# Performance work log

Measured on AMD Instinct MI355X. Metric: run time of the kernel, lower is better.

The kernel has to match this reference:

```python
import jax, jax.numpy as jnp
import numpy as np

D = 128        # node_state_dim
F = 10         # len(CHOSEN_CONNECTION_FEATURES)
N_IP = 20000
N_CONN = 100000
E = 200000
T = 3


def _seg_mean(vals, ids, n):
    s = jax.ops.segment_sum(vals, ids, num_segments=n)
    c = jax.ops.segment_sum(jnp.ones((vals.shape[0], 1), vals.dtype), ids, num_segments=n)
    return s / jnp.maximum(c, 1.0)


def _gru(x, h, kernel, rec_kernel, bias):
    # keras GRUCell, reset_after=True, gate order [z, r, hh]
    xm = x @ kernel + bias[0]
    hm = h @ rec_kernel + bias[1]
    xz, xr, xh = jnp.split(xm, 3, axis=-1)
    hz, hr, hh = jnp.split(hm, 3, axis=-1)
    z = jax.nn.sigmoid(xz + hz)
    r = jax.nn.sigmoid(xr + hr)
    hcand = jnp.tanh(xh + r * hh)
    return z * h + (1.0 - z) * hcand


def setup_inputs() -> dict:
    key = jax.random.key(0)
    ks = jax.random.split(key, 24)
    s = 0.02
    inp = {
        "feature_connection": jax.random.normal(ks[0], (N_CONN, F), jnp.float32),
        "src_ip_to_connection": jax.random.randint(ks[1], (E,), 0, N_IP, jnp.int32),
        "dst_ip_to_connection": jax.random.randint(ks[2], (E,), 0, N_CONN, jnp.int32),
        "src_connection_to_ip": jax.random.randint(ks[3], (E,), 0, N_CONN, jnp.int32),
        "dst_connection_to_ip": jax.random.randint(ks[4], (E,), 0, N_IP, jnp.int32),
        # message MLPs
        "W_m1": jax.random.normal(ks[5], (2 * D, D), jnp.float32) * s,
        "b_m1": jnp.zeros((D,), jnp.float32),
        "W_m2": jax.random.normal(ks[6], (2 * D, D), jnp.float32) * s,
        "b_m2": jnp.zeros((D,), jnp.float32),
        # GRU cells
        "gru_ip_k": jax.random.normal(ks[7], (D, 3 * D), jnp.float32) * s,
        "gru_ip_r": jax.random.normal(ks[8], (D, 3 * D), jnp.float32) * s,
        "gru_ip_b": jnp.zeros((2, 3 * D), jnp.float32),
        "gru_c_k": jax.random.normal(ks[9], (D, 3 * D), jnp.float32) * s,
        "gru_c_r": jax.random.normal(ks[10], (D, 3 * D), jnp.float32) * s,
        "gru_c_b": jnp.zeros((2, 3 * D), jnp.float32),
        # readout MLP
        "W_r1": jax.random.normal(ks[11], (D, 128), jnp.float32) * s,
        "b_r1": jnp.zeros((128,), jnp.float32),
        "W_r2": jax.random.normal(ks[12], (128, 64), jnp.float32) * s,
        "b_r2": jnp.zeros((64,), jnp.float32),
        "W_r3": jax.random.normal(ks[13], (64, 15), jnp.float32) * s,
        "b_r3": jnp.zeros((15,), jnp.float32),
    }
    return inp


def reference(feature_connection, src_ip_to_connection, dst_ip_to_connection,
              src_connection_to_ip, dst_connection_to_ip,
              W_m1, b_m1, W_m2, b_m2,
              gru_ip_k, gru_ip_r, gru_ip_b,
              gru_c_k, gru_c_r, gru_c_b,
              W_r1, b_r1, W_r2, b_r2, W_r3, b_r3):
    ip_state = jnp.ones((N_IP, D), jnp.float32)
    connection_state = jnp.concatenate(
        [feature_connection, jnp.zeros((N_CONN, D - F), jnp.float32)], axis=1)

    for _ in range(T):
        # ip -> connection messages
        nn_in = jnp.concatenate([ip_state[src_ip_to_connection],
                                 connection_state[dst_ip_to_connection]], axis=1)
        ip_message = jax.nn.relu(nn_in @ W_m1 + b_m1)            # [E, D]
        ip_mean = _seg_mean(ip_message, dst_ip_to_connection, N_CONN)
        # connection -> ip messages
        nn_in2 = jnp.concatenate([connection_state[src_connection_to_ip],
                                  ip_state[dst_connection_to_ip]], axis=1)
        conn_message = jax.nn.relu(nn_in2 @ W_m2 + b_m2)         # [E, D]
        conn_mean = _seg_mean(conn_message, dst_connection_to_ip, N_IP)
        # GRU updates
        ip_state = _gru(conn_mean, ip_state, gru_ip_k, gru_ip_r, gru_ip_b)
        connection_state = _gru(ip_mean, connection_state, gru_c_k, gru_c_r, gru_c_b)

    h = jax.nn.relu(connection_state @ W_r1 + b_r1)
    h = jax.nn.relu(h @ W_r2 + b_r2)
    return jax.nn.softmax(h @ W_r3 + b_r3, axis=-1)              # [N_CONN, 15]
```

## Files before the change

kernel.cpp:

```cpp
#include <hip/hip_runtime.h>
#include <math.h>

#define D 128
#define NF 10
#define N_IP 20000
#define N_CONN 100000
#define NE 200000
#define T_ROUNDS 3

typedef unsigned short u16;
using bf16x8 = __attribute__((ext_vector_type(8))) short;
using floatx4 = __attribute__((ext_vector_type(4))) float;

__device__ inline u16 f2bf(float f) {
  union { float f; unsigned u; } v; v.f = f;
  unsigned u = v.u;
  return (u16)((u + 0x7fffu + ((u >> 16) & 1u)) >> 16);
}
__device__ inline float bf2f(u16 h) {
  union { unsigned u; float f; } v; v.u = ((unsigned)h) << 16; return v.f;
}
__device__ __forceinline__ unsigned cvtpk(float lo, float hi) {
  unsigned r;
  asm("v_cvt_pk_bf16_f32 %0, %1, %2" : "=v"(r) : "v"(lo), "v"(hi));
  return r;
}

__device__ inline float fsigmoid(float s) { return 1.f / (1.f + __expf(-s)); }
__device__ inline float ftanh(float a) {
  a = fminf(fmaxf(a, -15.f), 15.f);
  float e = __expf(2.f * a);
  return (e - 1.f) / (e + 1.f);
}

__device__ __forceinline__ void gld16(const u16* g, u16* l) {
  __builtin_amdgcn_global_load_lds(
      (const __attribute__((address_space(1))) unsigned int*)g,
      (__attribute__((address_space(3))) unsigned int*)l, 16, 0, 0);
}

__global__ void k_setup(u16* __restrict__ ip_state, u16* __restrict__ conn_state,
                        const float* __restrict__ feat, int* __restrict__ cnt,
                        const float* __restrict__ gik, const float* __restrict__ gir,
                        const float* __restrict__ gck, const float* __restrict__ gcr,
                        const float* __restrict__ Wm1, const float* __restrict__ Wm2,
                        const float* __restrict__ Wr1, const float* __restrict__ Wr2,
                        u16* __restrict__ gikb, u16* __restrict__ girb,
                        u16* __restrict__ gckb, u16* __restrict__ gcrb,
                        u16* __restrict__ wm1b, u16* __restrict__ wm2b,
                        u16* __restrict__ wm1t, u16* __restrict__ wm2t,
                        u16* __restrict__ wr1b, u16* __restrict__ wr2b,
                        float* __restrict__ csum) {
  int i = blockIdx.x * blockDim.x + threadIdx.x;
  const int nip = N_IP * D;
  const int nstate = (N_IP + N_CONN) * D;
  if (i < nip) {
    ip_state[i] = 0x3F80;
  } else if (i < nstate) {
    int j = i - nip;
    int r = j >> 7, c = j & 127;
    conn_state[j] = (c < NF) ? f2bf(feat[r * NF + c]) : (u16)0;
  }
  if (i < N_CONN + N_IP) cnt[i] = 0;
  if (i < 196608) {
    int m = i / 49152, r = i % 49152;
    const float* W = (m == 0) ? gik : (m == 1) ? gir : (m == 2) ? gck : gcr;
    u16* Wb = (m == 0) ? gikb : (m == 1) ? girb : (m == 2) ? gckb : gcrb;
    int col = r >> 7, k = r & 127;
    Wb[r] = f2bf(W[k * 384 + col]);
  } else if (i < 278528) {
    int j = i - 196608;
    int m = j / 16384, r = j % 16384;
    const float* W; u16* Wb; int k0;
    if (m == 0) { W = Wm1; Wb = wm1b; k0 = 128; }
    else if (m == 1) { W = Wm2; Wb = wm2b; k0 = 128; }
    else if (m == 2) { W = Wm1; Wb = wm1t; k0 = 0; }
    else if (m == 3) { W = Wm2; Wb = wm2t; k0 = 0; }
    else { W = Wr1; Wb = wr1b; k0 = 0; }
    int col = r >> 7, k = r & 127;
    Wb[r] = f2bf(W[(k0 + k) * 128 + col]);
  } else if (i < 286720) {
    int r = i - 278528;
    int col = r >> 7, k = r & 127;
    wr2b[r] = f2bf(Wr2[k * 64 + col]);
  } else if (i < 286848) {
    int c = i - 286720;
    float s = 0.f;
    for (int k = 0; k < 128; k++) s += Wm1[k * 128 + c];
    csum[c] = s;
  }
}

__global__ void k_initP_count(const float* __restrict__ csum, const float* __restrict__ feat,
                              const float* __restrict__ Wm2,
                              u16* __restrict__ P1, u16* __restrict__ P2,
                              const int* __restrict__ d1, const int* __restrict__ d2,
                              int* __restrict__ c1, int* __restrict__ c2) {
  int i = blockIdx.x * blockDim.x + threadIdx.x;
  if (i < NE) {
    atomicAdd(&c1[d1[i]], 1);
    atomicAdd(&c2[d2[i]], 1);
  }
  const int n1 = N_IP * 16;
  const int n2 = N_CONN * 16;
  if (i < n1) {
    int r = i >> 4, g = i & 15;
    u16 v[8];
#pragma unroll
    for (int k = 0; k < 8; k++) v[k] = f2bf(csum[g * 8 + k]);
    *(uint4*)(P1 + (size_t)r * 128 + g * 8) = *(const uint4*)v;
  } else if (i < n1 + n2) {
    int j = i - n1;
    int r = j >> 4, g = j & 15;
    float acc[8] = {0.f, 0.f, 0.f, 0.f, 0.f, 0.f, 0.f, 0.f};
#pragma unroll
    for (int k = 0; k < NF; k++) {
      float f = feat[(size_t)r * NF + k];
      const float* wrow = Wm2 + (size_t)k * 128 + g * 8;
#pragma unroll
      for (int c = 0; c < 8; c++) acc[c] += f * wrow[c];
    }
    u16 v[8];
#pragma unroll
    for (int c = 0; c < 8; c++) v[c] = f2bf(acc[c]);
    *(uint4*)(P2 + (size_t)r * 128 + g * 8) = *(const uint4*)v;
  }
}

__global__ void k_scan_part2(const int* __restrict__ cnt1, int* __restrict__ bsum1,
                             int n1, int nb1,
                             const int* __restrict__ cnt2, int* __restrict__ bsum2, int n2) {
  const int* cnt; int* bsum; int n, b;
  if ((int)blockIdx.x < nb1) { cnt = cnt1; bsum = bsum1; n = n1; b = blockIdx.x; }
  else { cnt = cnt2; bsum = bsum2; n = n2; b = blockIdx.x - nb1; }
  int t = threadIdx.x;
  int base = b * 1024 + t * 4;
  int s = 0;
#pragma unroll
  for (int i = 0; i < 4; i++) { int j = base + i; if (j < n) s += cnt[j]; }
  for (int d = 32; d > 0; d >>= 1) s += __shfl_xor(s, d, 64);
  __shared__ int wred[4];
  int lane = t & 63, wv = t >> 6;
  if (lane == 0) wred[wv] = s;
  __syncthreads();
  if (t == 0) bsum[b] = wred[0] + wred[1] + wred[2] + wred[3];
}

__device__ inline void scan_mid_body(int* bsum, int m, int t) {
  int v = (t < m) ? bsum[t] : 0;
  int lane = t & 63, wv = t >> 6;
  int x = v;
  for (int d = 1; d < 64; d <<= 1) { int y = __shfl_up(x, d, 64); if (lane >= d) x += y; }
  __shared__ int wsum[4];
  if (lane == 63) wsum[wv] = x;
  __syncthreads();
  int add = 0;
  for (int i = 0; i < wv; i++) add += wsum[i];
  int ex = add + x - v;
  if (t < m) bsum[t] = ex;
  __syncthreads();
}

__global__ void k_scan_mid2(int* __restrict__ bsum1, int m1, int* __restrict__ bsum2, int m2) {
  int t = threadIdx.x;
  scan_mid_body(bsum1, m1, t);
  scan_mid_body(bsum2, m2, t);
}

__global__ void k_scan_final2(const int* __restrict__ cnt1, const int* __restrict__ bsum1,
                              int* __restrict__ off1, int* __restrict__ cur1, int n1, int nb1,
                              const int* __restrict__ cnt2, const int* __restrict__ bsum2,
                              int* __restrict__ off2, int* __restrict__ cur2, int n2) {
  const int* cnt; const int* bsum; int* off; int* cur; int n, b;
  if ((int)blockIdx.x < nb1) {
    cnt = cnt1; bsum = bsum1; off = off1; cur = cur1; n = n1; b = blockIdx.x;
  } else {
    cnt = cnt2; bsum = bsum2; off = off2; cur = cur2; n = n2; b = blockIdx.x - nb1;
  }
  int t = threadIdx.x;
  int base = b * 1024 + t * 4;
  int vals[4]; int s = 0;
#pragma unroll
  for (int i = 0; i < 4; i++) {
    int j = base + i;
    vals[i] = (j < n) ? cnt[j] : 0;
    s += vals[i];
  }
  int lane = t & 63, wv = t >> 6;
  int x = s;
  for (int d = 1; d < 64; d <<= 1) { int y = __shfl_up(x, d, 64); if (lane >= d) x += y; }
  __shared__ int wsum[4];
  if (lane == 63) wsum[wv] = x;
  __syncthreads();
  int add = 0;
  for (int i = 0; i < wv; i++) add += wsum[i];
  int run = add + x - s + bsum[b];
#pragma unroll
  for (int i = 0; i < 4; i++) {
    int j = base + i;
    if (j < n) { off[j] = run; cur[j] = run; }
    run += vals[i];
  }
}

__global__ void k_scatter(const int* __restrict__ s1, const int* __restrict__ d1,
                          const int* __restrict__ s2, const int* __restrict__ d2,
                          int* __restrict__ cur1, int* __restrict__ cur2,
                          int* __restrict__ o1, int* __restrict__ o2) {
  int e = blockIdx.x * blockDim.x + threadIdx.x;
  if (e >= NE) return;
  int p1 = atomicAdd(&cur1[d1[e]], 1);
  o1[p1] = s1[e];
  int p2 = atomicAdd(&cur2[d2[e]], 1);
  o2[p2] = s2[e];
}

__global__ __launch_bounds__(512, 4) void k_msggru(
    u16* __restrict__ st1, const u16* __restrict__ wq1, const float* __restrict__ qb1,
    const u16* __restrict__ P1g, const int* __restrict__ srcs1g,
    const int* __restrict__ off1g, const int* __restrict__ cnt1g,
    const u16* __restrict__ wx1, const u16* __restrict__ wh1, const float* __restrict__ gb1,
    const u16* __restrict__ wp1, u16* __restrict__ Pn1, int r1, int tiles1,
    u16* __restrict__ st2, const u16* __restrict__ wq2, const float* __restrict__ qb2,
    const u16* __restrict__ P2g, const int* __restrict__ srcs2g,
    const int* __restrict__ off2g, const int* __restrict__ cnt2g,
    const u16* __restrict__ wx2, const u16* __restrict__ wh2, const float* __restrict__ gb2,
    const u16* __restrict__ wp2, u16* __restrict__ Pn2, int r2, int doP) {
  __shared__ __align__(16) char smem[65536];
  u16* Wls = (u16*)smem;
  u16* Qb = (u16*)smem;
  u16* bufA = (u16*)smem;
  u16* bufB = (u16*)(smem + 12288);
  u16* Hls = (u16*)(smem + 32768);
  u16* H; const u16* Wqb; const float* qbias; const u16* P;
  const int* srcs; const int* off; const int* cnt;
  const u16* Wxb; const u16* Whb; const float* gbias;
  const u16* Wpt; u16* Pn; int rows, bm;
  if ((int)blockIdx.x < tiles1) {
    H = st1; Wqb = wq1; qbias = qb1; P = P1g; srcs = srcs1g; off = off1g; cnt = cnt1g;
    Wxb = wx1; Whb = wh1; gbias = gb1; Wpt = wp1; Pn = Pn1; rows = r1; bm = blockIdx.x * 128;
  } else {
    H = st2; Wqb = wq2; qbias = qb2; P = P2g; srcs = srcs2g; off = off2g; cnt = cnt2g;
    Wxb = wx2; Whb = wh2; gbias = gb2; Wpt = wp2; Pn = Pn2; rows = r2;
    bm = (blockIdx.x - tiles1) * 128;
  }
  const int tid = threadIdx.x, wv = tid >> 6, lane = tid & 63;
  const int lrow = lane & 15, quad = lane >> 4;
#pragma unroll
  for (int j = 0; j < 4; j++) {
    int c = j * 512 + tid;
    int row = c >> 4, sl = c & 15;
    gld16(Wqb + (size_t)row * 128 + ((sl ^ (row & 15)) * 8), Wls + (size_t)c * 8);
  }
#pragma unroll
  for (int i = 0; i < 4; i++) {
    int c = i * 512 + tid;
    int row = c >> 4, sl = c & 15;
    gld16(H + (size_t)(bm + row) * 128 + ((sl ^ (row & 15)) * 8), Hls + (size_t)c * 8);
  }
  int oArr[4], nArr[4];
#pragma unroll
  for (int it = 0; it < 4; it++) {
    int nl = (it * 512 + tid) >> 4;
    int node = bm + nl;
    oArr[it] = (node < rows) ? off[node] : 0;
    nArr[it] = (node < rows) ? cnt[node] : 0;
  }
  __syncthreads();
  bf16x8 ah[4];
#pragma unroll
  for (int ks = 0; ks < 4; ks++)
    ah[ks] = *(const bf16x8*)(Hls + (size_t)(wv * 16 + lrow) * 128 + (((ks * 4 + quad) ^ lrow) * 8));
  floatx4 acc[8];
#pragma unroll
  for (int ct = 0; ct < 8; ct++) acc[ct] = {0.f, 0.f, 0.f, 0.f};
#pragma unroll
  for (int ks = 0; ks < 4; ks++) {
#pragma unroll
    for (int ct = 0; ct < 8; ct++) {
      bf16x8 b = *(const bf16x8*)(Wls + (size_t)(ct * 16 + lrow) * 128 + (((4 * ks + quad) ^ lrow) * 8));
      acc[ct] = __builtin_amdgcn_mfma_f32_16x16x32_bf16(ah[ks], b, acc[ct], 0, 0, 0);
    }
  }
  __syncthreads();
  {
    const int lr = wv * 16 + quad * 4;
#pragma unroll
    for (int ct = 0; ct < 8; ct++) {
      int col = ct * 16 + lrow;
      float bv = qbias[col];
      unsigned p01 = cvtpk(acc[ct][0] + bv, acc[ct][1] + bv);
      unsigned p23 = cvtpk(acc[ct][2] + bv, acc[ct][3] + bv);
      Qb[(size_t)(lr + 0) * 128 + col] = (u16)p01;
      Qb[(size_t)(lr + 1) * 128 + col] = (u16)(p01 >> 16);
      Qb[(size_t)(lr + 2) * 128 + col] = (u16)p23;
      Qb[(size_t)(lr + 3) * 128 + col] = (u16)(p23 >> 16);
    }
  }
  __syncthreads();
#pragma unroll
  for (int it = 0; it < 4; it++) {
    int task = it * 512 + tid;
    int nl = task >> 4, g = task & 15;
    int node = bm + nl;
    if (node >= rows) continue;
    int c8 = g << 3;
    float q[8];
    {
      uint4 qv = *(const uint4*)(Qb + (size_t)nl * 128 + c8);
      unsigned qq[4] = {qv.x, qv.y, qv.z, qv.w};
#pragma unroll
      for (int k = 0; k < 4; k++) {
        q[2 * k] = __uint_as_float(qq[k] << 16);
        q[2 * k + 1] = __uint_as_float(qq[k] & 0xffff0000u);
      }
    }
    float acg[8] = {0.f, 0.f, 0.f, 0.f, 0.f, 0.f, 0.f, 0.f};
    int o = oArr[it], n = nArr[it];
    for (int i = 0; i < n; i += 4) {
      int rem = n - i;
      int s0 = srcs[o + i];
      int s1 = srcs[o + i + (rem > 1 ? 1 : 0)];
      int s2 = srcs[o + i + (rem > 2 ? 2 : 0)];
      int s3 = srcs[o + i + (rem > 3 ? 3 : 0)];
      uint4 v0 = *(const uint4*)(P + (size_t)s0 * 128 + c8);
      uint4 v1 = *(const uint4*)(P + (size_t)s1 * 128 + c8);
      uint4 v2 = *(const uint4*)(P + (size_t)s2 * 128 + c8);
      uint4 v3 = *(const uint4*)(P + (size_t)s3 * 128 + c8);
      unsigned w[16] = {v0.x, v0.y, v0.z, v0.w, v1.x, v1.y, v1.z, v1.w,
                        v2.x, v2.y, v2.z, v2.w, v3.x, v3.y, v3.z, v3.w};
#pragma unroll
      for (int e = 0; e < 4; e++) {
        bool val = (e == 0) || (rem > e);
#pragma unroll
        for (int k = 0; k < 4; k++) {
          unsigned ww = w[e * 4 + k];
          float lo = __uint_as_float(ww << 16);
          float hi = __uint_as_float(ww & 0xffff0000u);
          float t0 = fmaxf(lo + q[2 * k], 0.f);
          float t1 = fmaxf(hi + q[2 * k + 1], 0.f);
          if (val) { acg[2 * k] += t0; acg[2 * k + 1] += t1; }
        }
      }
    }
    float inv = 1.f / fmaxf((float)n, 1.f);
    uint4 ov;
    ov.x = cvtpk(acg[0] * inv, acg[1] * inv);
    ov.y = cvtpk(acg[2] * inv, acg[3] * inv);
    ov.z = cvtpk(acg[4] * inv, acg[5] * inv);
    ov.w = cvtpk(acg[6] * inv, acg[7] * inv);
    *(uint4*)(Qb + (size_t)nl * 128 + ((g ^ (nl & 15)) * 8)) = ov;
  }
  __syncthreads();
  bf16x8 ax[4];
#pragma unroll
  for (int ks = 0; ks < 4; ks++)
    ax[ks] = *(const bf16x8*)(Qb + (size_t)(wv * 16 + lrow) * 128 + (((ks * 4 + quad) ^ lrow) * 8));
  const int lr0 = wv * 16 + quad * 4;
  __syncthreads();
#pragma unroll
  for (int j = 0; j < 2; j++) {
    int c = j * 512 + tid;
    if (c < 768) {
      int gate = c >> 8, colw = (c >> 4) & 15, sl = c & 15;
      gld16(Wxb + (size_t)(gate * 128 + 0 * 16 + colw) * 128 + ((sl ^ colw) * 8),
            bufA + (size_t)c * 8);
    }
  }
  for (int ch = 0; ch < 8; ch++) {
    __syncthreads();
#pragma unroll
    for (int j = 0; j < 2; j++) {
      int c = j * 512 + tid;
      if (c < 768) {
        int gate = c >> 8, colw = (c >> 4) & 15, sl = c & 15;
        gld16(Whb + (size_t)(gate * 128 + ch * 16 + colw) * 128 + ((sl ^ colw) * 8),
              bufB + (size_t)c * 8);
      }
    }
    floatx4 gacc[3][2];
#pragma unroll
    for (int g = 0; g < 3; g++) {
      gacc[g][0] = {0.f, 0.f, 0.f, 0.f};
      gacc[g][1] = {0.f, 0.f, 0.f, 0.f};
    }
#pragma unroll
    for (int ks = 0; ks < 4; ks++) {
      int posu = ((4 * ks + quad) ^ lrow) * 8;
#pragma unroll
      for (int g = 0; g < 3; g++) {
        bf16x8 bx = *(const bf16x8*)(bufA + (size_t)(g * 16 + lrow) * 128 + posu);
        gacc[g][0] = __builtin_amdgcn_mfma_f32_16x16x32_bf16(ax[ks], bx, gacc[g][0], 0, 0, 0);
      }
    }
    __syncthreads();
    if (ch < 7) {
#pragma unroll
      for (int j = 0; j < 2; j++) {
        int c = j * 512 + tid;
        if (c < 768) {
          int gate = c >> 8, colw = (c >> 4) & 15, sl = c & 15;
          gld16(Wxb + (size_t)(gate * 128 + (ch + 1) * 16 + colw) * 128 + ((sl ^ colw) * 8),
                bufA + (size_t)c * 8);
        }
      }
    }
#pragma unroll
    for (int ks = 0; ks < 4; ks++) {
      int posu = ((4 * ks + quad) ^ lrow) * 8;
#pragma unroll
      for (int g = 0; g < 3; g++) {
        bf16x8 bh = *(const bf16x8*)(bufB + (size_t)(g * 16 + lrow) * 128 + posu);
        gacc[g][1] = __builtin_amdgcn_mfma_f32_16x16x32_bf16(ah[ks], bh, gacc[g][1], 0, 0, 0);
      }
    }
    int hcol = ch * 16 + lrow;
    float bxz = gbias[hcol];
    float bxr = gbias[128 + hcol];
    float bxh = gbias[256 + hcol];
    float bhz = gbias[384 + hcol];
    float bhr = gbias[384 + 128 + hcol];
    float bhh = gbias[384 + 256 + hcol];
    int ggr = 2 * ch + (lrow >> 3);
    int gel = lrow & 7;
    float hn[4];
#pragma unroll
    for (int reg = 0; reg < 4; reg++) {
      int lr = lr0 + reg;
      float xz = gacc[0][0][reg] + bxz;
      float xr = gacc[1][0][reg] + bxr;
      float xh = gacc[2][0][reg] + bxh;
      float hz = gacc[0][1][reg] + bhz;
      float hr = gacc[1][1][reg] + bhr;
      float hh = gacc[2][1][reg] + bhh;
      float z = fsigmoid(xz + hz);
      float rr = fsigmoid(xr + hr);
      float hc = ftanh(xh + rr * hh);
      const u16* hp = Hls + (size_t)lr * 128 + ((ggr ^ (lr & 15)) * 8) + gel;
      float hold = bf2f(*hp);
      hn[reg] = z * hold + (1.f - z) * hc;
    }
    unsigned q01 = cvtpk(hn[0], hn[1]);
    unsigned q23 = cvtpk(hn[2], hn[3]);
#define HPTR(R) (Hls + (size_t)(lr0 + (R)) * 128 + ((ggr ^ ((lr0 + (R)) & 15)) * 8) + gel)
    *HPTR(0) = (u16)q01;
    *HPTR(1) = (u16)(q01 >> 16);
    *HPTR(2) = (u16)q23;
    *HPTR(3) = (u16)(q23 >> 16);
#undef HPTR
  }
  __syncthreads();
#pragma unroll
  for (int i = 0; i < 4; i++) {
    int c = i * 512 + tid;
    int row = c >> 4, g = c & 15;
    int grow = bm + row;
    if (grow < rows)
      *(uint4*)(H + (size_t)grow * 128 + g * 8) =
          *(const uint4*)(Hls + (size_t)row * 128 + ((g ^ (row & 15)) * 8));
  }
  if (!doP) return;
  bf16x8 ah2[4];
#pragma unroll
  for (int ks = 0; ks < 4; ks++)
    ah2[ks] = *(const bf16x8*)(Hls + (size_t)(wv * 16 + lrow) * 128 + (((ks * 4 + quad) ^ lrow) * 8));
#pragma unroll
  for (int j = 0; j < 4; j++) {
    int c = j * 512 + tid;
    int row = c >> 4, sl = c & 15;
    gld16(Wpt + (size_t)row * 128 + ((sl ^ (row & 15)) * 8), Wls + (size_t)c * 8);
  }
  __syncthreads();
#pragma unroll
  for (int ct = 0; ct < 8; ct++) acc[ct] = {0.f, 0.f, 0.f, 0.f};
#pragma unroll
  for (int ks = 0; ks < 4; ks++) {
#pragma unroll
    for (int ct = 0; ct < 8; ct++) {
      bf16x8 b = *(const bf16x8*)(Wls + (size_t)(ct * 16 + lrow) * 128 + (((4 * ks + quad) ^ lrow) * 8));
      acc[ct] = __builtin_amdgcn_mfma_f32_16x16x32_bf16(ah2[ks], b, acc[ct], 0, 0, 0);
    }
  }
  u16* Cls = Hls;
  {
    const int lr = wv * 16 + quad * 4;
#pragma unroll
    for (int ct = 0; ct < 8; ct++) {
      int col = ct * 16 + lrow;
      unsigned p01 = cvtpk(acc[ct][0], acc[ct][1]);
      unsigned p23 = cvtpk(acc[ct][2], acc[ct][3]);
      Cls[(size_t)(lr + 0) * 128 + col] = (u16)p01;
      Cls[(size_t)(lr + 1) * 128 + col] = (u16)(p01 >> 16);
      Cls[(size_t)(lr + 2) * 128 + col] = (u16)p23;
      Cls[(size_t)(lr + 3) * 128 + col] = (u16)(p23 >> 16);
    }
  }
  __syncthreads();
#pragma unroll
  for (int i = 0; i < 4; i++) {
    int c = i * 512 + tid;
    int row = c >> 4, g = c & 15;
    int grow = bm + row;
    if (grow < rows)
      *(uint4*)(Pn + (size_t)grow * 128 + g * 8) =
          *(const uint4*)(Cls + (size_t)row * 128 + g * 8);
  }
}

__global__ __launch_bounds__(256, 4) void k_readout2(
    const u16* __restrict__ S, const u16* __restrict__ W1b, const float* __restrict__ b1,
    const u16* __restrict__ W2b, const float* __restrict__ b2,
    const float* __restrict__ W3, const float* __restrict__ b3,
    float* __restrict__ out, int M) {
  __shared__ __align__(16) char smem[33792];
  u16* Wls = (u16*)smem;
  u16* H1ls = (u16*)smem;
  u16* W2ls = (u16*)(smem + 17408);
  u16* H2ls = (u16*)smem;
  float* W3ls = (float*)(smem + 9216);
  float* b3ls = (float*)(smem + 9216 + 3840);
  const int tid = threadIdx.x, wv = tid >> 6, lane = tid & 63;
  const int lrow = lane & 15, quad = lane >> 4;
  const int slot = lane & 15;
  const int rowl = wv * 4 + (lane >> 4);
  const int bm = blockIdx.x * 64;
#pragma unroll
  for (int i = 0; i < 8; i++)
    gld16(W1b + (size_t)(i * 16 + rowl) * 128 + ((slot ^ rowl) * 8),
          Wls + (size_t)(i * 16 + wv * 4) * 128 + lane * 8);
  const int arow = bm + wv * 16 + lrow;
  const bool arv = arow < M;
  const bf16x8 zv = {0, 0, 0, 0, 0, 0, 0, 0};
  bf16x8 a[4];
#pragma unroll
  for (int ks = 0; ks < 4; ks++)
    a[ks] = arv ? *(const bf16x8*)(S + (size_t)arow * 128 + quad * 8 + ks * 32) : zv;
  __syncthreads();
  floatx4 acc1[8];
#pragma unroll
  for (int ct = 0; ct < 8; ct++) acc1[ct] = {0.f, 0.f, 0.f, 0.f};
#pragma unroll
  for (int ks = 0; ks < 4; ks++) {
#pragma unroll
    for (int ct = 0; ct < 8; ct++) {
      bf16x8 b = *(const bf16x8*)(Wls + (size_t)(ct * 16 + lrow) * 128 + (((4 * ks + quad) ^ lrow) * 8));
      acc1[ct] = __builtin_amdgcn_mfma_f32_16x16x32_bf16(a[ks], b, acc1[ct], 0, 0, 0);
    }
  }
  __syncthreads();
#pragma unroll
  for (int ct = 0; ct < 8; ct++) {
    int col = ct * 16 + lrow;
    float bv = b1[col];
#pragma unroll
    for (int reg = 0; reg < 4; reg++) {
      int lr = wv * 16 + quad * 4 + reg;
      H1ls[(size_t)lr * 136 + col] = f2bf(fmaxf(acc1[ct][reg] + bv, 0.f));
    }
  }
#pragma unroll
  for (int i = 0; i < 4; i++)
    gld16(W2b + (size_t)(i * 16 + rowl) * 128 + ((slot ^ rowl) * 8),
          W2ls + (size_t)(i * 16 + wv * 4) * 128 + lane * 8);
  __syncthreads();
  bf16x8 a2[4];
#pragma unroll
  for (int ks = 0; ks < 4; ks++)
    a2[ks] = *(const bf16x8*)(H1ls + (size_t)(wv * 16 + lrow) * 136 + quad * 8 + ks * 32);
  floatx4 acc2[4];
#pragma unroll
  for (int ct = 0; ct < 4; ct++) acc2[ct] = {0.f, 0.f, 0.f, 0.f};
#pragma unroll
  for (int ks = 0; ks < 4; ks++) {
#pragma unroll
    for (int ct = 0; ct < 4; ct++) {
      bf16x8 b = *(const bf16x8*)(W2ls + (size_t)(ct * 16 + lrow) * 128 + (((4 * ks + quad) ^ lrow) * 8));
      acc2[ct] = __builtin_amdgcn_mfma_f32_16x16x32_bf16(a2[ks], b, acc2[ct], 0, 0, 0);
    }
  }
  __syncthreads();
#pragma unroll
  for (int ct = 0; ct < 4; ct++) {
    int col = ct * 16 + lrow;
    float bv = b2[col];
#pragma unroll
    for (int reg = 0; reg < 4; reg++) {
      int lr = wv * 16 + quad * 4 + reg;
      H2ls[(size_t)lr * 72 + col] = f2bf(fmaxf(acc2[ct][reg] + bv, 0.f));
    }
  }
  for (int l = tid; l < 960; l += 256) W3ls[l] = W3[l];
  if (tid < 15) b3ls[tid] = b3[tid];
  __syncthreads();
  {
    int col = tid & 15;
    int rb = (tid >> 4) * 4;
    float lg[4] = {0.f, 0.f, 0.f, 0.f};
    if (col < 15) {
      float b3v = b3ls[col];
      lg[0] = b3v; lg[1] = b3v; lg[2] = b3v; lg[3] = b3v;
      for (int k8 = 0; k8 < 64; k8 += 8) {
        float w[8];
#pragma unroll
        for (int j = 0; j < 8; j++) w[j] = W3ls[(k8 + j) * 15 + col];
#pragma unroll
        for (int r = 0; r < 4; r++) {
          bf16x8 hv = *(const bf16x8*)(H2ls + (size_t)(rb + r) * 72 + k8);
#pragma unroll
          for (int j = 0; j < 8; j++) lg[r] += bf2f((u16)hv[j]) * w[j];
        }
      }
    }
#pragma unroll
    for (int r = 0; r < 4; r++) {
      float v = (col < 15) ? lg[r] : -3.0e38f;
      float m = v;
#pragma unroll
      for (int d = 1; d < 16; d <<= 1) m = fmaxf(m, __shfl_xor(m, d, 16));
      float e = (col < 15) ? __expf(lg[r] - m) : 0.f;
      float s = e;
#pragma unroll
      for (int d = 1; d < 16; d <<= 1) s += __shfl_xor(s, d, 16);
      int gr2 = bm + rb + r;
      if (col < 15 && gr2 < M) out[(size_t)gr2 * 15 + col] = e / s;
    }
  }
}

extern "C" void kernel_launch(void* const* d_in, const int* in_sizes, int n_in,
                              void* d_out, int out_size, void* d_ws, size_t ws_size,
                              hipStream_t stream) {
  const float* feat = (const float*)d_in[0];
  const int* src1 = (const int*)d_in[1];
  const int* dst1 = (const int*)d_in[2];
  const int* src2 = (const int*)d_in[3];
  const int* dst2 = (const int*)d_in[4];
  const float* Wm1 = (const float*)d_in[5];
  const float* bm1 = (const float*)d_in[6];
  const float* Wm2 = (const float*)d_in[7];
  const float* bm2 = (const float*)d_in[8];
  const float* gik = (const float*)d_in[9];
  const float* gir = (const float*)d_in[10];
  const float* gib = (const float*)d_in[11];
  const float* gck = (const float*)d_in[12];
  const float* gcr = (const float*)d_in[13];
  const float* gcb = (const float*)d_in[14];
  const float* Wr1 = (const float*)d_in[15];
  const float* br1 = (const float*)d_in[16];
  const float* Wr2 = (const float*)d_in[17];
  const float* br2 = (const float*)d_in[18];
  const float* Wr3 = (const float*)d_in[19];
  const float* br3 = (const float*)d_in[20];
  float* out = (float*)d_out;

  u16* w16 = (u16*)d_ws;
  size_t o = 0;
  u16* ip_state = w16 + o;   o += (size_t)N_IP * D;
  u16* conn_state = w16 + o; o += (size_t)N_CONN * D;
  u16* P1a = w16 + o;        o += (size_t)N_IP * D;
  u16* P2a = w16 + o;        o += (size_t)N_CONN * D;
  u16* P1b = w16 + o;        o += (size_t)N_IP * D;
  u16* P2b = w16 + o;        o += (size_t)N_CONN * D;
  u16* gikb = w16 + o;       o += 49152;
  u16* girb = w16 + o;       o += 49152;
  u16* gckb = w16 + o;       o += 49152;
  u16* gcrb = w16 + o;       o += 49152;
  u16* wm1b = w16 + o;       o += 16384;
  u16* wm2b = w16 + o;       o += 16384;
  u16* wm1t = w16 + o;       o += 16384;
  u16* wm2t = w16 + o;       o += 16384;
  u16* wr1b = w16 + o;       o += 16384;
  u16* wr2b = w16 + o;       o += 8192;
  float* csum = (float*)(w16 + o); o += 256;
  int* ip = (int*)(w16 + o);
  int* cnt1 = ip;  ip += N_CONN;
  int* cnt2 = ip;  ip += N_IP;
  int* off1 = ip;  ip += N_CONN;
  int* off2 = ip;  ip += N_IP;
  int* cur1 = ip;  ip += N_CONN;
  int* cur2 = ip;  ip += N_IP;
  int* srcs1 = ip; ip += NE;
  int* srcs2 = ip; ip += NE;
  int* bsum1 = ip; ip += 256;
  int* bsum2 = ip; ip += 256;

  const int BT = 256;

  const int nstate = (N_IP + N_CONN) * D;
  k_setup<<<(nstate + BT - 1) / BT, BT, 0, stream>>>(
      ip_state, conn_state, feat, cnt1,
      gik, gir, gck, gcr, Wm1, Wm2, Wr1, Wr2,
      gikb, girb, gckb, gcrb, wm1b, wm2b, wm1t, wm2t, wr1b, wr2b, csum);
  const int nPinit = (N_IP + N_CONN) * 16;
  k_initP_count<<<(nPinit + BT - 1) / BT, BT, 0, stream>>>(
      csum, feat, Wm2, P1a, P2a, dst1, dst2, cnt1, cnt2);

  const int nb1 = (N_CONN + 1023) / 1024, nb2 = (N_IP + 1023) / 1024;
  k_scan_part2<<<nb1 + nb2, 256, 0, stream>>>(cnt1, bsum1, N_CONN, nb1, cnt2, bsum2, N_IP);
  k_scan_mid2<<<1, 256, 0, stream>>>(bsum1, nb1, bsum2, nb2);
  k_scan_final2<<<nb1 + nb2, 256, 0, stream>>>(cnt1, bsum1, off1, cur1, N_CONN, nb1,
                                               cnt2, bsum2, off2, cur2, N_IP);
  k_scatter<<<(NE + BT - 1) / BT, BT, 0, stream>>>(src1, dst1, src2, dst2,
                                                   cur1, cur2, srcs1, srcs2);

  const int t128ip = (N_IP + 127) / 128;
  const int t128cn = (N_CONN + 127) / 128;
  const int t64cn = (N_CONN + 63) / 64;

  u16* P1buf[2] = {P1a, P1b};
  u16* P2buf[2] = {P2a, P2b};
  for (int t = 0; t < T_ROUNDS; t++) {
    int cu = t & 1, nx = cu ^ 1;
    k_msggru<<<t128ip + t128cn, 512, 0, stream>>>(
        ip_state, wm2b, bm2, P2buf[cu], srcs2, off2, cnt2, gikb, girb, gib,
        wm1t, P1buf[nx], N_IP, t128ip,
        conn_state, wm1b, bm1, P1buf[cu], srcs1, off1, cnt1, gckb, gcrb, gcb,
        wm2t, P2buf[nx], N_CONN, (t < T_ROUNDS - 1) ? 1 : 0);
  }

  k_readout2<<<t64cn, 256, 0, stream>>>(conn_state, wr1b, br1, wr2b, br2,
                                        Wr3, br3, out, N_CONN);
}
```

Baseline: 446.6 us.

## Fuse readout MLP into final GRU round and replace scan with atomic allocation

The three-kernel prefix scan for CSR offsets becomes a single kernel in which each block reserves its range with an atomicAdd on a global counter. This produces a valid but non-sorted bucket layout and removes two launches. The readout MLP and softmax are fused into the last msggru round for connection tiles, so the GRU output is reused from LDS instead of being re-read from global memory and a separate kernel launch is avoided. In exchange the fused kernel carries more code and parameters, and the atomic ordering makes the edge layout nondeterministic.

```diff
diff --git a/kernel.cpp b/kernel.cpp
--- a/kernel.cpp
+++ b/kernel.cpp
@@ -50,7 +50,7 @@
                         u16* __restrict__ wm1b, u16* __restrict__ wm2b,
                         u16* __restrict__ wm1t, u16* __restrict__ wm2t,
                         u16* __restrict__ wr1b, u16* __restrict__ wr2b,
-                        float* __restrict__ csum) {
+                        float* __restrict__ csum, int* __restrict__ gctr) {
   int i = blockIdx.x * blockDim.x + threadIdx.x;
   const int nip = N_IP * D;
   const int nstate = (N_IP + N_CONN) * D;
@@ -62,6 +62,7 @@
     conn_state[j] = (c < NF) ? f2bf(feat[r * NF + c]) : (u16)0;
   }
   if (i < N_CONN + N_IP) cnt[i] = 0;
+  if (i < 2) gctr[i] = 0;
   if (i < 196608) {
     int m = i / 49152, r = i % 49152;
     const float* W = (m == 0) ? gik : (m == 1) ? gir : (m == 2) ? gck : gcr;
@@ -127,55 +128,15 @@
   }
 }
 
-__global__ void k_scan_part2(const int* __restrict__ cnt1, int* __restrict__ bsum1,
-                             int n1, int nb1,
-                             const int* __restrict__ cnt2, int* __restrict__ bsum2, int n2) {
-  const int* cnt; int* bsum; int n, b;
-  if ((int)blockIdx.x < nb1) { cnt = cnt1; bsum = bsum1; n = n1; b = blockIdx.x; }
-  else { cnt = cnt2; bsum = bsum2; n = n2; b = blockIdx.x - nb1; }
-  int t = threadIdx.x;
-  int base = b * 1024 + t * 4;
-  int s = 0;
-#pragma unroll
-  for (int i = 0; i < 4; i++) { int j = base + i; if (j < n) s += cnt[j]; }
-  for (int d = 32; d > 0; d >>= 1) s += __shfl_xor(s, d, 64);
-  __shared__ int wred[4];
-  int lane = t & 63, wv = t >> 6;
-  if (lane == 0) wred[wv] = s;
-  __syncthreads();
-  if (t == 0) bsum[b] = wred[0] + wred[1] + wred[2] + wred[3];
-}
-
-__device__ inline void scan_mid_body(int* bsum, int m, int t) {
-  int v = (t < m) ? bsum[t] : 0;
-  int lane = t & 63, wv = t >> 6;
-  int x = v;
-  for (int d = 1; d < 64; d <<= 1) { int y = __shfl_up(x, d, 64); if (lane >= d) x += y; }
-  __shared__ int wsum[4];
-  if (lane == 63) wsum[wv] = x;
-  __syncthreads();
-  int add = 0;
-  for (int i = 0; i < wv; i++) add += wsum[i];
-  int ex = add + x - v;
-  if (t < m) bsum[t] = ex;
-  __syncthreads();
-}
-
-__global__ void k_scan_mid2(int* __restrict__ bsum1, int m1, int* __restrict__ bsum2, int m2) {
-  int t = threadIdx.x;
-  scan_mid_body(bsum1, m1, t);
-  scan_mid_body(bsum2, m2, t);
-}
-
-__global__ void k_scan_final2(const int* __restrict__ cnt1, const int* __restrict__ bsum1,
-                              int* __restrict__ off1, int* __restrict__ cur1, int n1, int nb1,
-                              const int* __restrict__ cnt2, const int* __restrict__ bsum2,
-                              int* __restrict__ off2, int* __restrict__ cur2, int n2) {
-  const int* cnt; const int* bsum; int* off; int* cur; int n, b;
+__global__ void k_alloc(const int* __restrict__ cnt1, int* __restrict__ off1,
+                        int* __restrict__ cur1, int n1, int nb1,
+                        const int* __restrict__ cnt2, int* __restrict__ off2,
+                        int* __restrict__ cur2, int n2, int* __restrict__ gctr) {
+  const int* cnt; int* off; int* cur; int n, b; int* g;
   if ((int)blockIdx.x < nb1) {
-    cnt = cnt1; bsum = bsum1; off = off1; cur = cur1; n = n1; b = blockIdx.x;
+    cnt = cnt1; off = off1; cur = cur1; n = n1; b = blockIdx.x; g = gctr;
   } else {
-    cnt = cnt2; bsum = bsum2; off = off2; cur = cur2; n = n2; b = blockIdx.x - nb1;
+    cnt = cnt2; off = off2; cur = cur2; n = n2; b = blockIdx.x - nb1; g = gctr + 1;
   }
   int t = threadIdx.x;
   int base = b * 1024 + t * 4;
@@ -190,11 +151,14 @@
   int x = s;
   for (int d = 1; d < 64; d <<= 1) { int y = __shfl_up(x, d, 64); if (lane >= d) x += y; }
   __shared__ int wsum[4];
+  __shared__ int gbase;
   if (lane == 63) wsum[wv] = x;
   __syncthreads();
   int add = 0;
   for (int i = 0; i < wv; i++) add += wsum[i];
-  int run = add + x - s + bsum[b];
+  if (t == 0) gbase = atomicAdd(g, wsum[0] + wsum[1] + wsum[2] + wsum[3]);
+  __syncthreads();
+  int run = gbase + add + x - s;
 #pragma unroll
   for (int i = 0; i < 4; i++) {
     int j = base + i;
@@ -225,7 +189,11 @@
     const u16* __restrict__ P2g, const int* __restrict__ srcs2g,
     const int* __restrict__ off2g, const int* __restrict__ cnt2g,
     const u16* __restrict__ wx2, const u16* __restrict__ wh2, const float* __restrict__ gb2,
-    const u16* __restrict__ wp2, u16* __restrict__ Pn2, int r2, int doP) {
+    const u16* __restrict__ wp2, u16* __restrict__ Pn2, int r2, int doP,
+    const u16* __restrict__ w1r, const float* __restrict__ b1r,
+    const u16* __restrict__ w2r, const float* __restrict__ b2r,
+    const float* __restrict__ W3r, const float* __restrict__ b3r,
+    float* __restrict__ outp, int doRd) {
   __shared__ __align__(16) char smem[65536];
   u16* Wls = (u16*)smem;
   u16* Qb = (u16*)smem;
@@ -236,7 +204,8 @@
   const int* srcs; const int* off; const int* cnt;
   const u16* Wxb; const u16* Whb; const float* gbias;
   const u16* Wpt; u16* Pn; int rows, bm;
-  if ((int)blockIdx.x < tiles1) {
+  const bool side2 = (int)blockIdx.x >= tiles1;
+  if (!side2) {
     H = st1; Wqb = wq1; qbias = qb1; P = P1g; srcs = srcs1g; off = off1g; cnt = cnt1g;
     Wxb = wx1; Whb = wh1; gbias = gb1; Wpt = wp1; Pn = Pn1; rows = r1; bm = blockIdx.x * 128;
   } else {
@@ -459,16 +428,64 @@
       *(uint4*)(H + (size_t)grow * 128 + g * 8) =
           *(const uint4*)(Hls + (size_t)row * 128 + ((g ^ (row & 15)) * 8));
   }
-  if (!doP) return;
-  bf16x8 ah2[4];
+  if (doP) {
+    bf16x8 ah2[4];
+#pragma unroll
+    for (int ks = 0; ks < 4; ks++)
+      ah2[ks] = *(const bf16x8*)(Hls + (size_t)(wv * 16 + lrow) * 128 + (((ks * 4 + quad) ^ lrow) * 8));
+#pragma unroll
+    for (int j = 0; j < 4; j++) {
+      int c = j * 512 + tid;
+      int row = c >> 4, sl = c & 15;
+      gld16(Wpt + (size_t)row * 128 + ((sl ^ (row & 15)) * 8), Wls + (size_t)c * 8);
+    }
+    __syncthreads();
+#pragma unroll
+    for (int ct = 0; ct < 8; ct++) acc[ct] = {0.f, 0.f, 0.f, 0.f};
+#pragma unroll
+    for (int ks = 0; ks < 4; ks++) {
+#pragma unroll
+      for (int ct = 0; ct < 8; ct++) {
+        bf16x8 b = *(const bf16x8*)(Wls + (size_t)(ct * 16 + lrow) * 128 + (((4 * ks + quad) ^ lrow) * 8));
+        acc[ct] = __builtin_amdgcn_mfma_f32_16x16x32_bf16(ah2[ks], b, acc[ct], 0, 0, 0);
+      }
+    }
+    u16* Cls = Hls;
+    {
+      const int lr = wv * 16 + quad * 4;
+#pragma unroll
+      for (int ct = 0; ct < 8; ct++) {
+        int col = ct * 16 + lrow;
+        unsigned p01 = cvtpk(acc[ct][0], acc[ct][1]);
+        unsigned p23 = cvtpk(acc[ct][2], acc[ct][3]);
+        Cls[(size_t)(lr + 0) * 128 + col] = (u16)p01;
+        Cls[(size_t)(lr + 1) * 128 + col] = (u16)(p01 >> 16);
+        Cls[(size_t)(lr + 2) * 128 + col] = (u16)p23;
+        Cls[(size_t)(lr + 3) * 128 + col] = (u16)(p23 >> 16);
+      }
+    }
+    __syncthreads();
+#pragma unroll
+    for (int i = 0; i < 4; i++) {
+      int c = i * 512 + tid;
+      int row = c >> 4, g = c & 15;
+      int grow = bm + row;
+      if (grow < rows)
+        *(uint4*)(Pn + (size_t)grow * 128 + g * 8) =
+            *(const uint4*)(Cls + (size_t)row * 128 + g * 8);
+    }
+    return;
+  }
+  if (!doRd || !side2) return;
+  bf16x8 ar[4];
 #pragma unroll
   for (int ks = 0; ks < 4; ks++)
-    ah2[ks] = *(const bf16x8*)(Hls + (size_t)(wv * 16 + lrow) * 128 + (((ks * 4 + quad) ^ lrow) * 8));
+    ar[ks] = *(const bf16x8*)(Hls + (size_t)(wv * 16 + lrow) * 128 + (((ks * 4 + quad) ^ lrow) * 8));
 #pragma unroll
   for (int j = 0; j < 4; j++) {
     int c = j * 512 + tid;
     int row = c >> 4, sl = c & 15;
-    gld16(Wpt + (size_t)row * 128 + ((sl ^ (row & 15)) * 8), Wls + (size_t)c * 8);
+    gld16(w1r + (size_t)row * 128 + ((sl ^ (row & 15)) * 8), Wls + (size_t)c * 8);
   }
   __syncthreads();
 #pragma unroll
@@ -478,95 +495,36 @@
 #pragma unroll
     for (int ct = 0; ct < 8; ct++) {
       bf16x8 b = *(const bf16x8*)(Wls + (size_t)(ct * 16 + lrow) * 128 + (((4 * ks + quad) ^ lrow) * 8));
-      acc[ct] = __builtin_amdgcn_mfma_f32_16x16x32_bf16(ah2[ks], b, acc[ct], 0, 0, 0);
-    }
-  }
-  u16* Cls = Hls;
-  {
-    const int lr = wv * 16 + quad * 4;
-#pragma unroll
-    for (int ct = 0; ct < 8; ct++) {
-      int col = ct * 16 + lrow;
-      unsigned p01 = cvtpk(acc[ct][0], acc[ct][1]);
-      unsigned p23 = cvtpk(acc[ct][2], acc[ct][3]);
-      Cls[(size_t)(lr + 0) * 128 + col] = (u16)p01;
-      Cls[(size_t)(lr + 1) * 128 + col] = (u16)(p01 >> 16);
-      Cls[(size_t)(lr + 2) * 128 + col] = (u16)p23;
-      Cls[(size_t)(lr + 3) * 128 + col] = (u16)(p23 >> 16);
-    }
-  }
-  __syncthreads();
-#pragma unroll
-  for (int i = 0; i < 4; i++) {
-    int c = i * 512 + tid;
-    int row = c >> 4, g = c & 15;
-    int grow = bm + row;
-    if (grow < rows)
-      *(uint4*)(Pn + (size_t)grow * 128 + g * 8) =
-          *(const uint4*)(Cls + (size_t)row * 128 + g * 8);
-  }
-}
-
-__global__ __launch_bounds__(256, 4) void k_readout2(
-    const u16* __restrict__ S, const u16* __restrict__ W1b, const float* __restrict__ b1,
-    const u16* __restrict__ W2b, const float* __restrict__ b2,
-    const float* __restrict__ W3, const float* __restrict__ b3,
-    float* __restrict__ out, int M) {
-  __shared__ __align__(16) char smem[33792];
-  u16* Wls = (u16*)smem;
-  u16* H1ls = (u16*)smem;
-  u16* W2ls = (u16*)(smem + 17408);
-  u16* H2ls = (u16*)smem;
-  float* W3ls = (float*)(smem + 9216);
-  float* b3ls = (float*)(smem + 9216 + 3840);
-  const int tid = threadIdx.x, wv = tid >> 6, lane = tid & 63;
-  const int lrow = lane & 15, quad = lane >> 4;
-  const int slot = lane & 15;
-  const int rowl = wv * 4 + (lane >> 4);
-  const int bm = blockIdx.x * 64;
-#pragma unroll
-  for (int i = 0; i < 8; i++)
-    gld16(W1b + (size_t)(i * 16 + rowl) * 128 + ((slot ^ rowl) * 8),
-          Wls + (size_t)(i * 16 + wv * 4) * 128 + lane * 8);
-  const int arow = bm + wv * 16 + lrow;
-  const bool arv = arow < M;
-  const bf16x8 zv = {0, 0, 0, 0, 0, 0, 0, 0};
-  bf16x8 a[4];
-#pragma unroll
-  for (int ks = 0; ks < 4; ks++)
-    a[ks] = arv ? *(const bf16x8*)(S + (size_t)arow * 128 + quad * 8 + ks * 32) : zv;
-  __syncthreads();
-  floatx4 acc1[8];
-#pragma unroll
-  for (int ct = 0; ct < 8; ct++) acc1[ct] = {0.f, 0.f, 0.f, 0.f};
-#pragma unroll
-  for (int ks = 0; ks < 4; ks++) {
-#pragma unroll
-    for (int ct = 0; ct < 8; ct++) {
-      bf16x8 b = *(const bf16x8*)(Wls + (size_t)(ct * 16 + lrow) * 128 + (((4 * ks + quad) ^ lrow) * 8));
-      acc1[ct] = __builtin_amdgcn_mfma_f32_16x16x32_bf16(a[ks], b, acc1[ct], 0, 0, 0);
-    }
-  }
-  __syncthreads();
+      acc[ct] = __builtin_amdgcn_mfma_f32_16x16x32_bf16(ar[ks], b, acc[ct], 0, 0, 0);
+    }
+  }
 #pragma unroll
   for (int ct = 0; ct < 8; ct++) {
     int col = ct * 16 + lrow;
-    float bv = b1[col];
-#pragma unroll
-    for (int reg = 0; reg < 4; reg++) {
-      int lr = wv * 16 + quad * 4 + reg;
-      H1ls[(size_t)lr * 136 + col] = f2bf(fmaxf(acc1[ct][reg] + bv, 0.f));
-    }
-  }
-#pragma unroll
-  for (int i = 0; i < 4; i++)
-    gld16(W2b + (size_t)(i * 16 + rowl) * 128 + ((slot ^ rowl) * 8),
-          W2ls + (size_t)(i * 16 + wv * 4) * 128 + lane * 8);
+    float bv = b1r[col];
+    int ggr = 2 * ct + (lrow >> 3);
+    int gel = lrow & 7;
+    unsigned p01 = cvtpk(fmaxf(acc[ct][0] + bv, 0.f), fmaxf(acc[ct][1] + bv, 0.f));
+    unsigned p23 = cvtpk(fmaxf(acc[ct][2] + bv, 0.f), fmaxf(acc[ct][3] + bv, 0.f));
+#define H1PTR(R) (Hls + (size_t)(lr0 + (R)) * 128 + ((ggr ^ ((lr0 + (R)) & 15)) * 8) + gel)
+    *H1PTR(0) = (u16)p01;
+    *H1PTR(1) = (u16)(p01 >> 16);
+    *H1PTR(2) = (u16)p23;
+    *H1PTR(3) = (u16)(p23 >> 16);
+#undef H1PTR
+  }
+  __syncthreads();
+#pragma unroll
+  for (int j = 0; j < 2; j++) {
+    int c = j * 512 + tid;
+    int row = c >> 4, sl = c & 15;
+    gld16(w2r + (size_t)row * 128 + ((sl ^ (row & 15)) * 8), Wls + (size_t)c * 8);
+  }
   __syncthreads();
   bf16x8 a2[4];
 #pragma unroll
   for (int ks = 0; ks < 4; ks++)
-    a2[ks] = *(const bf16x8*)(H1ls + (size_t)(wv * 16 + lrow) * 136 + quad * 8 + ks * 32);
+    a2[ks] = *(const bf16x8*)(Hls + (size_t)(wv * 16 + lrow) * 128 + (((ks * 4 + quad) ^ lrow) * 8));
   floatx4 acc2[4];
 #pragma unroll
   for (int ct = 0; ct < 4; ct++) acc2[ct] = {0.f, 0.f, 0.f, 0.f};
@@ -574,23 +532,24 @@
   for (int ks = 0; ks < 4; ks++) {
 #pragma unroll
     for (int ct = 0; ct < 4; ct++) {
-      bf16x8 b = *(const bf16x8*)(W2ls + (size_t)(ct * 16 + lrow) * 128 + (((4 * ks + quad) ^ lrow) * 8));
+      bf16x8 b = *(const bf16x8*)(Wls + (size_t)(ct * 16 + lrow) * 128 + (((4 * ks + quad) ^ lrow) * 8));
       acc2[ct] = __builtin_amdgcn_mfma_f32_16x16x32_bf16(a2[ks], b, acc2[ct], 0, 0, 0);
     }
   }
   __syncthreads();
+  u16* H2 = (u16*)smem;
+  float* W3ls = (float*)(smem + 18432);
+  float* b3ls = (float*)(smem + 18432 + 3840);
 #pragma unroll
   for (int ct = 0; ct < 4; ct++) {
     int col = ct * 16 + lrow;
-    float bv = b2[col];
-#pragma unroll
-    for (int reg = 0; reg < 4; reg++) {
-      int lr = wv * 16 + quad * 4 + reg;
-      H2ls[(size_t)lr * 72 + col] = f2bf(fmaxf(acc2[ct][reg] + bv, 0.f));
-    }
-  }
-  for (int l = tid; l < 960; l += 256) W3ls[l] = W3[l];
-  if (tid < 15) b3ls[tid] = b3[tid];
+    float bv = b2r[col];
+#pragma unroll
+    for (int reg = 0; reg < 4; reg++)
+      H2[(size_t)(lr0 + reg) * 72 + col] = f2bf(fmaxf(acc2[ct][reg] + bv, 0.f));
+  }
+  for (int l = tid; l < 960; l += 512) W3ls[l] = W3r[l];
+  if (tid < 15) b3ls[tid] = b3r[tid];
   __syncthreads();
   {
     int col = tid & 15;
@@ -605,7 +564,7 @@
         for (int j = 0; j < 8; j++) w[j] = W3ls[(k8 + j) * 15 + col];
 #pragma unroll
         for (int r = 0; r < 4; r++) {
-          bf16x8 hv = *(const bf16x8*)(H2ls + (size_t)(rb + r) * 72 + k8);
+          bf16x8 hv = *(const bf16x8*)(H2 + (size_t)(rb + r) * 72 + k8);
 #pragma unroll
           for (int j = 0; j < 8; j++) lg[r] += bf2f((u16)hv[j]) * w[j];
         }
@@ -622,7 +581,7 @@
 #pragma unroll
       for (int d = 1; d < 16; d <<= 1) s += __shfl_xor(s, d, 16);
       int gr2 = bm + rb + r;
-      if (col < 15 && gr2 < M) out[(size_t)gr2 * 15 + col] = e / s;
+      if (col < 15 && gr2 < rows) outp[(size_t)gr2 * 15 + col] = e / s;
     }
   }
 }
@@ -681,8 +640,7 @@
   int* cur2 = ip;  ip += N_IP;
   int* srcs1 = ip; ip += NE;
   int* srcs2 = ip; ip += NE;
-  int* bsum1 = ip; ip += 256;
-  int* bsum2 = ip; ip += 256;
+  int* gctr = ip;  ip += 8;
 
   const int BT = 256;
 
@@ -690,34 +648,30 @@
   k_setup<<<(nstate + BT - 1) / BT, BT, 0, stream>>>(
       ip_state, conn_state, feat, cnt1,
       gik, gir, gck, gcr, Wm1, Wm2, Wr1, Wr2,
-      gikb, girb, gckb, gcrb, wm1b, wm2b, wm1t, wm2t, wr1b, wr2b, csum);
+      gikb, girb, gckb, gcrb, wm1b, wm2b, wm1t, wm2t, wr1b, wr2b, csum, gctr);
   const int nPinit = (N_IP + N_CONN) * 16;
   k_initP_count<<<(nPinit + BT - 1) / BT, BT, 0, stream>>>(
       csum, feat, Wm2, P1a, P2a, dst1, dst2, cnt1, cnt2);
 
   const int nb1 = (N_CONN + 1023) / 1024, nb2 = (N_IP + 1023) / 1024;
-  k_scan_part2<<<nb1 + nb2, 256, 0, stream>>>(cnt1, bsum1, N_CONN, nb1, cnt2, bsum2, N_IP);
-  k_scan_mid2<<<1, 256, 0, stream>>>(bsum1, nb1, bsum2, nb2);
-  k_scan_final2<<<nb1 + nb2, 256, 0, stream>>>(cnt1, bsum1, off1, cur1, N_CONN, nb1,
-                                               cnt2, bsum2, off2, cur2, N_IP);
+  k_alloc<<<nb1 + nb2, 256, 0, stream>>>(cnt1, off1, cur1, N_CONN, nb1,
+                                         cnt2, off2, cur2, N_IP, gctr);
   k_scatter<<<(NE + BT - 1) / BT, BT, 0, stream>>>(src1, dst1, src2, dst2,
                                                    cur1, cur2, srcs1, srcs2);
 
   const int t128ip = (N_IP + 127) / 128;
   const int t128cn = (N_CONN + 127) / 128;
-  const int t64cn = (N_CONN + 63) / 64;
 
   u16* P1buf[2] = {P1a, P1b};
   u16* P2buf[2] = {P2a, P2b};
   for (int t = 0; t < T_ROUNDS; t++) {
     int cu = t & 1, nx = cu ^ 1;
+    int last = (t == T_ROUNDS - 1);
     k_msggru<<<t128ip + t128cn, 512, 0, stream>>>(
         ip_state, wm2b, bm2, P2buf[cu], srcs2, off2, cnt2, gikb, girb, gib,
         wm1t, P1buf[nx], N_IP, t128ip,
         conn_state, wm1b, bm1, P1buf[cu], srcs1, off1, cnt1, gckb, gcrb, gcb,
-        wm2t, P2buf[nx], N_CONN, (t < T_ROUNDS - 1) ? 1 : 0);
-  }
-
-  k_readout2<<<t64cn, 256, 0, stream>>>(conn_state, wr1b, br1, wr2b, br2,
-                                        Wr3, br3, out, N_CONN);
-}
+        wm2t, P2buf[nx], N_CONN, last ? 0 : 1,
+        wr1b, br1, wr2b, br2, Wr3, br3, out, last ? 1 : 0);
+  }
+}
```

Measured after the change: 435.3 us. 2.5% less time.
